# Kernel tuning notes

Measured on AMD Instinct MI355X. Metric: run time of the kernel, lower is better.

Reference implementation:

```python
import jax, jax.numpy as jnp
import numpy as np

NUM_ENT = 14541; NUM_REL = 237; NUM_EDGES = 544230
D = 200; B = 2048
IPERM = 1; IK_H = 20; IK_W = 10; NFILT = 96; KER = 9
FLAT = IK_H * 2 * IK_W * NFILT * IPERM
LEAKY = 0.2; EPS = 1e-5


def _chequer_perm(rng):
    # faithful reimplementation of RagatInteractE.get_chequer_perm
    ent_perm = np.stack([rng.permutation(D) for _ in range(IPERM)])
    rel_perm = np.stack([rng.permutation(D) for _ in range(IPERM)])
    comb = []
    for k in range(IPERM):
        temp = []; ei = 0; ri = 0
        for i in range(IK_H):
            for j in range(IK_W):
                ent_first = (k % 2 == 0) == (i % 2 == 0)
                if ent_first:
                    temp.append(ent_perm[k, ei]); ei += 1
                    temp.append(rel_perm[k, ri] + D); ri += 1
                else:
                    temp.append(rel_perm[k, ri] + D); ri += 1
                    temp.append(ent_perm[k, ei]); ei += 1
        comb.append(temp)
    return jnp.asarray(np.asarray(comb, dtype=np.int32))


def _bn1d(x, g, b):  # [N, C], training-mode batch stats (torch default)
    m = x.mean(0); v = x.var(0)
    return (x - m) / jnp.sqrt(v + EPS) * g + b


def _bn2d(x, g, b):  # [N, C, H, W]
    m = x.mean((0, 2, 3), keepdims=True); v = x.var((0, 2, 3), keepdims=True)
    return (x - m) / jnp.sqrt(v + EPS) * g[None, :, None, None] + b[None, :, None, None]


def _seg_softmax_agg(score, msg, seg, n):
    # segment softmax over edges grouped by destination node, then weighted scatter-add
    mx = jax.ops.segment_max(score, seg, num_segments=n)
    ex = jnp.exp(score - mx[seg])
    den = jax.ops.segment_sum(ex, seg, num_segments=n)
    alpha = ex / (den[seg] + 1e-16)
    return jax.ops.segment_sum(msg * alpha[:, None], seg, num_segments=n)


def setup_inputs() -> dict:
    key = jax.random.key(0)
    ks = jax.random.split(key, 20)
    f = lambda k, shp, s=0.1: jax.random.normal(k, shp, jnp.float32) * s
    rng = np.random.RandomState(0)
    return {
        'init_embed': f(ks[0], (NUM_ENT, D)),
        'init_rel': f(ks[1], (2 * NUM_REL, D)),
        'loop_rel': f(ks[2], (1, D)),
        'w_in': f(ks[3], (D, D)),
        'w_out': f(ks[4], (D, D)),
        'w_loop': f(ks[5], (D, D)),
        'w_rel': f(ks[6], (D, D)),
        'att_in': f(ks[7], (D,)),
        'att_out': f(ks[8], (D,)),
        'bn_conv_g': jnp.ones((D,), jnp.float32),
        'bn_conv_b': jnp.zeros((D,), jnp.float32),
        'conv_filt': f(ks[9], (NFILT, 1, KER, KER)),
        'bn0_g': jnp.ones((IPERM,), jnp.float32),
        'bn0_b': jnp.zeros((IPERM,), jnp.float32),
        'bn1_g': jnp.ones((NFILT * IPERM,), jnp.float32),
        'bn1_b': jnp.zeros((NFILT * IPERM,), jnp.float32),
        'fc_w': f(ks[10], (FLAT, D), 0.02),
        'fc_b': jnp.zeros((D,), jnp.float32),
        'bn2_g': jnp.ones((D,), jnp.float32),
        'bn2_b': jnp.zeros((D,), jnp.float32),
        'bias': jnp.zeros((NUM_ENT,), jnp.float32),
        'edge_index': jax.random.randint(ks[11], (2, NUM_EDGES), 0, NUM_ENT, jnp.int32),
        'edge_type': jnp.concatenate([
            jax.random.randint(ks[12], (NUM_EDGES // 2,), 0, NUM_REL, jnp.int32),
            jax.random.randint(ks[13], (NUM_EDGES // 2,), NUM_REL, 2 * NUM_REL, jnp.int32)]),
        'sub': jax.random.randint(ks[14], (B,), 0, NUM_ENT, jnp.int32),
        'rel': jax.random.randint(ks[15], (B,), 0, 2 * NUM_REL, jnp.int32),
        'chequer_perm': _chequer_perm(rng),
    }


def reference(init_embed, init_rel, loop_rel, w_in, w_out, w_loop, w_rel,
              att_in, att_out, bn_conv_g, bn_conv_b, conv_filt,
              bn0_g, bn0_b, bn1_g, bn1_b, fc_w, fc_b, bn2_g, bn2_b, bias,
              edge_index, edge_type, sub, rel, chequer_perm):
    # --- RagatConv (1 layer): relation-aware composition + edge attention + scatter-agg ---
    rel_full = jnp.concatenate([init_rel, loop_rel], 0)
    src, dst = edge_index[0], edge_index[1]
    comp = init_embed[dst] * rel_full[edge_type]          # [E, D] mult composition
    half = NUM_EDGES // 2
    msg_in = comp[:half] @ w_in                           # [E/2, D]
    msg_out = comp[half:] @ w_out
    s_in = jax.nn.leaky_relu((msg_in * att_in).sum(-1), LEAKY)
    s_out = jax.nn.leaky_relu((msg_out * att_out).sum(-1), LEAKY)
    agg_in = _seg_softmax_agg(s_in, msg_in, src[:half], NUM_ENT)
    agg_out = _seg_softmax_agg(s_out, msg_out, src[half:], NUM_ENT)
    loop_msg = (init_embed * loop_rel[0]) @ w_loop
    ent = (agg_in + agg_out + loop_msg) / 3.0
    ent = jnp.tanh(_bn1d(ent, bn_conv_g, bn_conv_b))      # [num_ent, D]
    rel_out = init_rel @ w_rel                            # [2*num_rel, D]

    # --- InteractE chequer-perm circular-conv scoring ---
    comb = jnp.concatenate([ent[sub], rel_out[rel]], 1)   # [B, 2D]
    cheq = comb[:, chequer_perm]                          # [B, IPERM, 2D]
    x = cheq.reshape(B, IPERM, 2 * IK_W, IK_H)
    x = _bn2d(x, bn0_g, bn0_b)
    p = KER // 2
    x = jnp.concatenate([x[..., -p:, :], x, x[..., :p, :]], axis=2)  # circular pad H
    x = jnp.concatenate([x[..., -p:], x, x[..., :p]], axis=3)        # circular pad W
    kern = jnp.tile(conv_filt, (IPERM, 1, 1, 1))          # [NFILT*IPERM, 1, K, K]
    x = jax.lax.conv_general_dilated(x, kern, (1, 1), 'VALID',
                                     dimension_numbers=('NCHW', 'OIHW', 'NCHW'),
                                     feature_group_count=IPERM)       # [B, 96, 20, 20]
    x = jax.nn.relu(_bn2d(x, bn1_g, bn1_b))
    x = x.reshape(B, FLAT)
    x = x @ fc_w + fc_b
    x = jax.nn.relu(_bn1d(x, bn2_g, bn2_b))               # [B, D]
    scores = x @ ent.T + bias                              # one_to_n scoring
    return jax.nn.sigmoid(scores)
```

## Files before the change

### kernel.cpp

```cpp
#include <hip/hip_runtime.h>
#include <hip/hip_bf16.h>

constexpr int DV     = 200;
constexpr int N_ENT  = 14541;
constexpr int N_EDGE = 544230;
constexpr int HALF_E = N_EDGE / 2;
constexpr int NSEG   = 2 * N_ENT;
constexpr int BB     = 2048;
constexpr int NF     = 96;
constexpr int FLATN  = 38400;
constexpr float LEAK = 0.2f;
constexpr float BEPS = 1e-5f;

typedef unsigned int u32;
typedef unsigned short u16;
typedef __attribute__((ext_vector_type(8))) short bf16x8;
typedef __attribute__((ext_vector_type(4))) float f32x4;
typedef __attribute__((ext_vector_type(4))) unsigned short u16x4;

constexpr size_t OFF_S    = 0;
constexpr size_t OFF_EID  = 544230;
constexpr size_t OFF_CNT  = 1088460;
constexpr size_t OFF_OFFS = 1117542;
constexpr size_t OFF_AGG  = 1146624;
constexpr size_t OFF_FC   = 6963218;
constexpr size_t ZERO_BEG = OFF_CNT;
constexpr size_t ZERO_END = OFF_FC + 409600;
constexpr size_t OFF_V    = 7372818;
constexpr size_t OFF_WTH  = 0;
constexpr size_t OFF_ENTH = 3840000;
constexpr size_t OFF_ENTL = 5352264;
constexpr size_t OFF_WTL  = 7373220;
constexpr size_t OFF_EMB  = 7373218;
constexpr size_t OFF_EPRE = 10281418;
constexpr size_t OFF_ENT  = 13189618;
constexpr size_t OFF_RELO = 16097818;
constexpr size_t OFF_CM   = 16192618;
constexpr size_t OFF_CV   = 16192818;
constexpr size_t OFF_CHEQ = 16193018;
constexpr size_t OFF_YH   = 16193020;
constexpr size_t OFF_YL   = 16406012;
constexpr size_t OFF_P0   = 17012218;
constexpr size_t OFF_ST0  = 17016314;
constexpr size_t OFF_CHP  = 17016316;
constexpr size_t OFF_B1SC = 17409532;
constexpr size_t OFF_B1BI = 17409628;
constexpr size_t OFF_XC   = 17819324;
constexpr size_t WS_WORDS = OFF_XC + 39321600;

__device__ inline float bf2f(u16 u) { return __uint_as_float(((u32)u) << 16); }
__device__ inline u16 f2bf(float f) {
    __hip_bfloat16 h = __float2bfloat16(f);
    return *reinterpret_cast<u16*>(&h);
}
__device__ inline void gl_lds16(const void* g, void* l) {
    __builtin_amdgcn_global_load_lds(
        (const __attribute__((address_space(1))) void*)g,
        (__attribute__((address_space(3))) void*)l, 16, 0, 0);
}

__global__ void k_vatt(const float* __restrict__ w_in, const float* __restrict__ w_out,
                       const float* __restrict__ att_in, const float* __restrict__ att_out,
                       float* __restrict__ v) {
    int t = blockIdx.x * 256 + threadIdx.x;
    if (t < DV) {
        float s = 0.f;
        for (int j = 0; j < DV; ++j) s += w_in[t * DV + j] * att_in[j];
        v[t] = s;
    } else if (t < 2 * DV) {
        int k = t - DV;
        float s = 0.f;
        for (int j = 0; j < DV; ++j) s += w_out[k * DV + j] * att_out[j];
        v[t] = s;
    }
}

__global__ void k_edge_score(const float* __restrict__ embed, const float* __restrict__ rel,
                             const int* __restrict__ eidx, const int* __restrict__ etype,
                             const float* __restrict__ v, float* __restrict__ s_all) {
    int gw = (blockIdx.x * 256 + threadIdx.x) >> 6;
    int lane = threadIdx.x & 63;
    if (gw >= N_EDGE) return;
    int e = gw;
    int dst = eidx[N_EDGE + e], et = etype[e];
    int dir = (e >= HALF_E);
    const float* vv = v + dir * DV;
    const float* er = embed + (size_t)dst * DV;
    const float* rr = rel + (size_t)et * DV;
    float acc = 0.f;
    for (int d = lane; d < DV; d += 64) acc += er[d] * rr[d] * vv[d];
    for (int off = 32; off > 0; off >>= 1) acc += __shfl_down(acc, off);
    if (lane == 0) {
        float s = acc > 0.f ? acc : LEAK * acc;
        s_all[e] = s;
    }
}

__global__ void k_hist(const int* __restrict__ eidx, u32* __restrict__ cnt) {
    int e = blockIdx.x * 256 + threadIdx.x;
    if (e >= N_EDGE) return;
    int seg = (e >= HALF_E ? N_ENT : 0) + eidx[e];
    atomicAdd(&cnt[seg], 1u);
}

__global__ void k_scan(u32* __restrict__ cnt, u32* __restrict__ offs) {
    __shared__ u32 s[256];
    __shared__ u32 base;
    if (threadIdx.x == 0) base = 0;
    __syncthreads();
    for (int c0 = 0; c0 < NSEG; c0 += 256) {
        int i = c0 + threadIdx.x;
        u32 vv = (i < NSEG) ? cnt[i] : 0;
        s[threadIdx.x] = vv;
        __syncthreads();
        for (int o = 1; o < 256; o <<= 1) {
            u32 t = (threadIdx.x >= (u32)o) ? s[threadIdx.x - o] : 0u;
            __syncthreads();
            s[threadIdx.x] += t;
            __syncthreads();
        }
        u32 exc = base + s[threadIdx.x] - vv;
        if (i < NSEG) { offs[i] = exc; cnt[i] = exc; }
        __syncthreads();
        if (threadIdx.x == 255) base += s[255];
        __syncthreads();
    }
}

__global__ void k_scatter(const int* __restrict__ eidx, u32* __restrict__ pos,
                          u32* __restrict__ eid) {
    int e = blockIdx.x * 256 + threadIdx.x;
    if (e >= N_EDGE) return;
    int seg = (e >= HALF_E ? N_ENT : 0) + eidx[e];
    u32 slot = atomicAdd(&pos[seg], 1u);
    eid[slot] = (u32)e;
}

__global__ void k_seg_agg(const float* __restrict__ embed, const float* __restrict__ rel,
                          const int* __restrict__ eidx, const int* __restrict__ etype,
                          const float* __restrict__ s_all, const u32* __restrict__ offs,
                          const u32* __restrict__ eid, float* __restrict__ aggC) {
    int gw = (blockIdx.x * 256 + threadIdx.x) >> 6;
    int lane = threadIdx.x & 63;
    if (gw >= NSEG) return;
    u32 beg = offs[gw];
    u32 end = (gw == NSEG - 1) ? (u32)N_EDGE : offs[gw + 1];
    int deg = (int)(end - beg);
    if (deg == 0) return;
    float m = -1e30f;
    for (int i = lane; i < deg; i += 64) m = fmaxf(m, s_all[eid[beg + i]]);
    for (int o = 32; o > 0; o >>= 1) m = fmaxf(m, __shfl_xor(m, o));
    float dsum = 0.f;
    for (int i = lane; i < deg; i += 64) dsum += expf(s_all[eid[beg + i]] - m);
    for (int o = 32; o > 0; o >>= 1) dsum += __shfl_xor(dsum, o);
    float inv = 1.f / (dsum + 1e-16f);
    float a0 = 0.f, a1 = 0.f, a2 = 0.f, a3 = 0.f;
    bool t3 = (lane < 8);
    for (int j = 0; j < deg; ++j) {
        int e = (int)eid[beg + j];
        float alpha = expf(s_all[e] - m) * inv;
        int dst = eidx[N_EDGE + e], et = etype[e];
        const float* er = embed + (size_t)dst * DV;
        const float* rr = rel + (size_t)et * DV;
        float p0 = er[lane] * rr[lane];
        float p1 = er[lane + 64] * rr[lane + 64];
        float p2 = er[lane + 128] * rr[lane + 128];
        float p3 = t3 ? er[lane + 192] * rr[lane + 192] : 0.f;
        a0 = fmaf(p0, alpha, a0);
        a1 = fmaf(p1, alpha, a1);
        a2 = fmaf(p2, alpha, a2);
        a3 = fmaf(p3, alpha, a3);
    }
    float* ag = aggC + (size_t)gw * DV;
    ag[lane] = a0;
    ag[lane + 64] = a1;
    ag[lane + 128] = a2;
    if (t3) ag[lane + 192] = a3;
}

__global__ void k_embloop(const float* __restrict__ embed, const float* __restrict__ lr,
                          float* __restrict__ outp) {
    size_t i = (size_t)blockIdx.x * 256 + threadIdx.x;
    if (i < (size_t)N_ENT * DV) outp[i] = embed[i] * lr[i % DV];
}

__global__ void gemm_nn(const float* __restrict__ A, const float* __restrict__ B,
                        float* __restrict__ C, int M, int N, int K, int beta) {
    __shared__ float As[16][65];
    __shared__ float Bs[16][64];
    int bm = blockIdx.x * 64, bn = blockIdx.y * 64;
    int tx = threadIdx.x & 15, ty = threadIdx.x >> 4;
    float acc[4][4] = {};
    for (int k0 = 0; k0 < K; k0 += 16) {
        for (int i = threadIdx.x; i < 1024; i += 256) {
            int m = i >> 4, k = i & 15;
            int gm = bm + m, gk = k0 + k;
            As[k][m] = (gm < M && gk < K) ? A[(size_t)gm * K + gk] : 0.f;
        }
        for (int i = threadIdx.x; i < 1024; i += 256) {
            int k = i >> 6, n = i & 63;
            int gk = k0 + k, gn = bn + n;
            Bs[k][n] = (gk < K && gn < N) ? B[(size_t)gk * N + gn] : 0.f;
        }
        __syncthreads();
#pragma unroll
        for (int k = 0; k < 16; ++k) {
            float a[4], bv[4];
#pragma unroll
            for (int i = 0; i < 4; i++) a[i] = As[k][ty * 4 + i];
#pragma unroll
            for (int j = 0; j < 4; j++) bv[j] = Bs[k][tx * 4 + j];
#pragma unroll
            for (int i = 0; i < 4; i++)
#pragma unroll
                for (int j = 0; j < 4; j++) acc[i][j] += a[i] * bv[j];
        }
        __syncthreads();
    }
#pragma unroll
    for (int i = 0; i < 4; i++) {
        int r = bm + ty * 4 + i;
        if (r >= M) continue;
#pragma unroll
        for (int j = 0; j < 4; j++) {
            int c = bn + tx * 4 + j;
            if (c >= N) continue;
            size_t idx = (size_t)r * N + c;
            C[idx] = beta ? C[idx] + acc[i][j] : acc[i][j];
        }
    }
}

__global__ void k_colstats(const float* __restrict__ X, int R,
                           float* __restrict__ cm, float* __restrict__ cv) {
    int col = blockIdx.x;
    __shared__ float rs[256], rss[256];
    float s = 0.f, ss = 0.f;
    for (int r = threadIdx.x; r < R; r += 256) {
        float x = X[(size_t)r * DV + col];
        s += x; ss += x * x;
    }
    rs[threadIdx.x] = s; rss[threadIdx.x] = ss;
    __syncthreads();
    for (int o = 128; o > 0; o >>= 1) {
        if (threadIdx.x < o) { rs[threadIdx.x] += rs[threadIdx.x + o]; rss[threadIdx.x] += rss[threadIdx.x + o]; }
        __syncthreads();
    }
    if (threadIdx.x == 0) {
        float m = rs[0] / R;
        cm[col] = m;
        cv[col] = rss[0] / R - m * m;
    }
}

__global__ void k_bn_ent(const float* __restrict__ epre, const float* __restrict__ cm,
                         const float* __restrict__ cv, const float* __restrict__ g,
                         const float* __restrict__ b, float* __restrict__ ent,
                         u16* __restrict__ eh, u16* __restrict__ el) {
    size_t i = (size_t)blockIdx.x * 256 + threadIdx.x;
    if (i >= (size_t)N_ENT * 208) return;
    int row = (int)(i / 208), col = (int)(i % 208);
    if (col < DV) {
        float val = (epre[(size_t)row * DV + col] - cm[col]) * rsqrtf(cv[col] + 9.f * BEPS) * g[col] + b[col];
        val = tanhf(val);
        ent[(size_t)row * DV + col] = val;
        u16 h = f2bf(val);
        eh[i] = h;
        el[i] = f2bf(val - bf2f(h));
    } else { eh[i] = 0; el[i] = 0; }
}

__global__ void k_bn2y(const float* __restrict__ fc, const float* __restrict__ cm,
                       const float* __restrict__ cv, const float* __restrict__ g,
                       const float* __restrict__ b, u16* __restrict__ yh,
                       u16* __restrict__ yl) {
    size_t i = (size_t)blockIdx.x * 256 + threadIdx.x;
    if (i >= (size_t)BB * 208) return;
    int row = (int)(i / 208), col = (int)(i % 208);
    if (col < DV) {
        float val = (fc[(size_t)row * DV + col] - cm[col]) * rsqrtf(cv[col] + BEPS) * g[col] + b[col];
        val = fmaxf(val, 0.f);
        u16 h = f2bf(val);
        yh[i] = h;
        yl[i] = f2bf(val - bf2f(h));
    } else { yh[i] = 0; yl[i] = 0; }
}

__global__ __launch_bounds__(256) void k_wt(const float* __restrict__ W,
                                            u16* __restrict__ Wth, u16* __restrict__ Wtl) {
    __shared__ float lds[64][65];
    int k0 = blockIdx.x * 64, n0 = blockIdx.y * 64;
    for (int idx = threadIdx.x; idx < 4096; idx += 256) {
        int kl = idx >> 6, nl = idx & 63;
        int gk = k0 + kl, gn = n0 + nl;
        lds[kl][nl] = (gn < DV) ? W[(size_t)gk * DV + gn] : 0.f;
    }
    __syncthreads();
    int nl = threadIdx.x >> 2, kq = threadIdx.x & 3;
    int gn = n0 + nl;
    if (gn >= DV) return;
    size_t base = (size_t)gn * FLATN + k0 + kq * 16;
    bf16x8 vh0, vh1, vl0, vl1;
#pragma unroll
    for (int j = 0; j < 8; ++j) {
        float w0 = lds[kq * 16 + j][nl];
        u16 h0 = f2bf(w0);
        vh0[j] = (short)h0; vl0[j] = (short)f2bf(w0 - bf2f(h0));
        float w1 = lds[kq * 16 + 8 + j][nl];
        u16 h1 = f2bf(w1);
        vh1[j] = (short)h1; vl1[j] = (short)f2bf(w1 - bf2f(h1));
    }
    *reinterpret_cast<bf16x8*>(Wth + base)     = vh0;
    *reinterpret_cast<bf16x8*>(Wth + base + 8) = vh1;
    *reinterpret_cast<bf16x8*>(Wtl + base)     = vl0;
    *reinterpret_cast<bf16x8*>(Wtl + base + 8) = vl1;
}

__global__ void k_cheq(const float* __restrict__ ent, const float* __restrict__ rel_out,
                       const int* __restrict__ sub, const int* __restrict__ rel,
                       const int* __restrict__ perm, float* __restrict__ cheq,
                       float* __restrict__ p0) {
    int b = blockIdx.x;
    int sb = sub[b], rb = rel[b];
    __shared__ float rs[256], rss[256];
    float s = 0.f, ss = 0.f;
    for (int i = threadIdx.x; i < 400; i += 256) {
        int p = perm[i];
        float v = (p < DV) ? ent[(size_t)sb * DV + p] : rel_out[(size_t)rb * DV + (p - DV)];
        cheq[(size_t)b * 400 + i] = v;
        s += v; ss += v * v;
    }
    rs[threadIdx.x] = s; rss[threadIdx.x] = ss;
    __syncthreads();
    for (int o = 128; o > 0; o >>= 1) {
        if (threadIdx.x < o) { rs[threadIdx.x] += rs[threadIdx.x + o]; rss[threadIdx.x] += rss[threadIdx.x + o]; }
        __syncthreads();
    }
    if (threadIdx.x == 0) { p0[b] = rs[0]; p0[BB + b] = rss[0]; }
}

__global__ void k_red_bn0(const float* __restrict__ p0, float* __restrict__ st) {
    __shared__ float rs[256], rss[256];
    float s = 0.f, ss = 0.f;
    for (int i = threadIdx.x; i < BB; i += 256) { s += p0[i]; ss += p0[BB + i]; }
    rs[threadIdx.x] = s; rss[threadIdx.x] = ss;
    __syncthreads();
    for (int o = 128; o > 0; o >>= 1) {
        if (threadIdx.x < o) { rs[threadIdx.x] += rs[threadIdx.x + o]; rss[threadIdx.x] += rss[threadIdx.x + o]; }
        __syncthreads();
    }
    if (threadIdx.x == 0) { st[0] = rs[0]; st[1] = rss[0]; }
}

__global__ __launch_bounds__(192, 3) void k_conv(const float* __restrict__ cheq,
                                              const float* __restrict__ st,
                                              const float* __restrict__ g0, const float* __restrict__ b0,
                                              const float* __restrict__ filt,
                                              __hip_bfloat16* __restrict__ xconv,
                                              float* __restrict__ chp) {
    int b = blockIdx.x, t = threadIdx.x;
    __shared__ float pad[784];
    __shared__ float flds[7968];
    __shared__ float red[192];
    for (int i = t; i < 7776; i += 192) {
        int f = i / 81, q = i - f * 81;
        flds[f * 83 + q] = filt[i];
    }
    const float N0 = (float)BB * 400.f;
    float m = st[0] / N0;
    float va = st[1] / N0 - m * m;
    float sg = rsqrtf(va + BEPS) * g0[0];
    float sb = b0[0] - m * sg;
    for (int i = t; i < 784; i += 192) {
        int h = i / 28, w = i % 28;
        int r = (h + 16) % 20, c = (w + 16) % 20;
        pad[i] = cheq[(size_t)b * 400 + r * 20 + c] * sg + sb;
    }
    __syncthreads();
    int f = t % 96, hp = t / 96;
    const float* fbase = flds + f * 83;
    float cs = 0.f, css = 0.f;
    u16* xo = (u16*)xconv + (size_t)b * FLATN + f * 400 + hp * 200;
    for (int rt = 0; rt < 10; ++rt) {
        int y = hp * 10 + rt;
        float acc[20];
#pragma unroll
        for (int x = 0; x < 20; ++x) acc[x] = 0.f;
        for (int dy = 0; dy < 9; ++dy) {
            float pr[28];
            const float4* prow = reinterpret_cast<const float4*>(&pad[(y + dy) * 28]);
#pragma unroll
            for (int qv = 0; qv < 7; ++qv) {
                float4 v4 = prow[qv];
                pr[qv * 4 + 0] = v4.x; pr[qv * 4 + 1] = v4.y;
                pr[qv * 4 + 2] = v4.z; pr[qv * 4 + 3] = v4.w;
            }
            float fw[9];
#pragma unroll
            for (int dx = 0; dx < 9; ++dx) fw[dx] = fbase[dy * 9 + dx];
#pragma unroll
            for (int dx = 0; dx < 9; ++dx)
#pragma unroll
                for (int x = 0; x < 20; ++x)
                    acc[x] = fmaf(pr[x + dx], fw[dx], acc[x]);
        }
#pragma unroll
        for (int x = 0; x < 20; ++x) { cs += acc[x]; css += acc[x] * acc[x]; }
#pragma unroll
        for (int jj = 0; jj < 5; ++jj) {
            u16x4 o;
#pragma unroll
            for (int q2 = 0; q2 < 4; ++q2) o[q2] = f2bf(acc[jj * 4 + q2]);
            *reinterpret_cast<u16x4*>(xo + rt * 20 + jj * 4) = o;
        }
    }
    red[t] = cs; __syncthreads();
    if (t < 96) chp[(size_t)b * 192 + t] = red[t] + red[t + 96];
    __syncthreads();
    red[t] = css; __syncthreads();
    if (t < 96) chp[(size_t)b * 192 + 96 + t] = red[t] + red[t + 96];
}

__global__ void k_bn1_final(const float* __restrict__ chp, const float* __restrict__ g1,
                            const float* __restrict__ b1, float* __restrict__ sc,
                            float* __restrict__ bi) {
    int c = blockIdx.x;
    __shared__ float rs[256], rss[256];
    float s = 0.f, ss = 0.f;
    for (int b = threadIdx.x; b < BB; b += 256) {
        s += chp[(size_t)b * 192 + c];
        ss += chp[(size_t)b * 192 + 96 + c];
    }
    rs[threadIdx.x] = s; rss[threadIdx.x] = ss;
    __syncthreads();
    for (int o = 128; o > 0; o >>= 1) {
        if (threadIdx.x < o) { rs[threadIdx.x] += rs[threadIdx.x + o]; rss[threadIdx.x] += rss[threadIdx.x + o]; }
        __syncthreads();
    }
    if (threadIdx.x == 0) {
        float N = (float)BB * 400.f;
        float m = rs[0] / N;
        float v = rss[0] / N - m * m;
        float s_ = rsqrtf(v + BEPS) * g1[c];
        sc[c] = s_;
        bi[c] = b1[c] - m * s_;
    }
}

__global__ __launch_bounds__(256) void k_fc_mfma(const u16* __restrict__ X,
        const u16* __restrict__ Wth, const u16* __restrict__ Wtl,
        const float* __restrict__ sc, const float* __restrict__ bi,
        float* __restrict__ outp) {
    __shared__ __align__(16) char blds[53248];
    int tid = threadIdx.x;
    int w = tid >> 6, lane = tid & 63;
    int lrow = lane & 15, lkg = lane >> 4;
    int mw = blockIdx.x * 128 + w * 32;
    int kbase = blockIdx.y * 1280;
    f32x4 acc[2][13] = {};
    for (int it = 0; it < 20; ++it) {
        int k0 = kbase + it * 64;
        __syncthreads();
        bf16x8 araw[2][2];
#pragma unroll
        for (int mf = 0; mf < 2; ++mf)
#pragma unroll
            for (int kt = 0; kt < 2; ++kt) {
                int r = mw + mf * 16 + lrow;
                int kk = k0 + kt * 32 + lkg * 8;
                araw[mf][kt] = *reinterpret_cast<const bf16x8*>(X + (size_t)r * FLATN + kk);
            }
#pragma unroll
        for (int q = 0; q < 7; ++q) {
            int bidx = q * 256 + w * 64;
            if (bidx < 1600) {
                int idx = bidx + lane;
                int n = idx >> 3;
                int slot = (idx & 7) ^ (n & 7);
                size_t gsrc = (size_t)n * FLATN + k0 + slot * 8;
                gl_lds16(Wth + gsrc, blds + bidx * 16);
                gl_lds16(Wtl + gsrc, blds + 26624 + bidx * 16);
            }
        }
        bf16x8 ah[2][2], al[2][2];
#pragma unroll
        for (int mf = 0; mf < 2; ++mf)
#pragma unroll
            for (int kt = 0; kt < 2; ++kt) {
                int kk = k0 + kt * 32 + lkg * 8;
                int c = kk / 400;
                float s_ = sc[c], b_ = bi[c];
                bf16x8 fh, fl;
#pragma unroll
                for (int j = 0; j < 8; ++j) {
                    float v = bf2f((u16)araw[mf][kt][j]);
                    v = fmaxf(fmaf(v, s_, b_), 0.f);
                    u16 h = f2bf(v);
                    fh[j] = (short)h;
                    fl[j] = (short)f2bf(v - bf2f(h));
                }
                ah[mf][kt] = fh;
                al[mf][kt] = fl;
            }
        __syncthreads();
#pragma unroll
        for (int nt = 0; nt < 13; ++nt) {
            int n = nt * 16 + lrow;
            int row = n * 128, nx = n & 7;
            int off0 = row + ((lkg ^ nx) << 4);
            int off1 = row + (((4 + lkg) ^ nx) << 4);
            bf16x8 bh0 = *reinterpret_cast<const bf16x8*>(blds + off0);
            bf16x8 bh1 = *reinterpret_cast<const bf16x8*>(blds + off1);
            bf16x8 bl0 = *reinterpret_cast<const bf16x8*>(blds + 26624 + off0);
            bf16x8 bl1 = *reinterpret_cast<const bf16x8*>(blds + 26624 + off1);
#pragma unroll
            for (int mf = 0; mf < 2; ++mf) {
                acc[mf][nt] = __builtin_amdgcn_mfma_f32_16x16x32_bf16(ah[mf][0], bh0, acc[mf][nt], 0, 0, 0);
                acc[mf][nt] = __builtin_amdgcn_mfma_f32_16x16x32_bf16(ah[mf][1], bh1, acc[mf][nt], 0, 0, 0);
                acc[mf][nt] = __builtin_amdgcn_mfma_f32_16x16x32_bf16(ah[mf][0], bl0, acc[mf][nt], 0, 0, 0);
                acc[mf][nt] = __builtin_amdgcn_mfma_f32_16x16x32_bf16(ah[mf][1], bl1, acc[mf][nt], 0, 0, 0);
                acc[mf][nt] = __builtin_amdgcn_mfma_f32_16x16x32_bf16(al[mf][0], bh0, acc[mf][nt], 0, 0, 0);
                acc[mf][nt] = __builtin_amdgcn_mfma_f32_16x16x32_bf16(al[mf][1], bh1, acc[mf][nt], 0, 0, 0);
            }
        }
    }
#pragma unroll
    for (int mf = 0; mf < 2; ++mf)
#pragma unroll
        for (int nt = 0; nt < 13; ++nt) {
            int col = nt * 16 + lrow;
            if (col < DV) {
#pragma unroll
                for (int i = 0; i < 4; ++i) {
                    int r = mw + mf * 16 + lkg * 4 + i;
                    unsafeAtomicAdd(&outp[(size_t)r * DV + col], acc[mf][nt][i]);
                }
            }
        }
}

__global__ __launch_bounds__(256) void k_sc_mfma(const u16* __restrict__ Yh, const u16* __restrict__ Yl,
        const u16* __restrict__ Eh, const u16* __restrict__ El,
        const float* __restrict__ bias, float* __restrict__ outp) {
    __shared__ __align__(16) char elds[32768];
    int tid = threadIdx.x;
    int w = tid >> 6, lane = tid & 63;
    int lrow = lane & 15, lkg = lane >> 4;
    int mw = blockIdx.x * 128 + w * 32;
    int bn = blockIdx.y * 256;
    f32x4 acc[2][16] = {};
    bf16x8 zv = {};
    for (int kt = 0; kt < 7; ++kt) {
        int kbase = kt * 32;
        __syncthreads();
        int kk = kbase + lkg * 8;
        bool kval = (kt < 6) || (lkg < 2);
        bf16x8 ah[2], al[2];
#pragma unroll
        for (int mf = 0; mf < 2; ++mf) {
            int r = mw + mf * 16 + lrow;
            size_t off = (size_t)r * 208 + kk;
            ah[mf] = kval ? *reinterpret_cast<const bf16x8*>(Yh + off) : zv;
            al[mf] = kval ? *reinterpret_cast<const bf16x8*>(Yl + off) : zv;
        }
#pragma unroll
        for (int q = 0; q < 4; ++q) {
            int bidx = q * 256 + w * 64;
            int idx = bidx + lane;
            int n = idx >> 2;
            int slot = (idx & 3) ^ (n & 3);
            int gn = bn + n; if (gn > N_ENT - 1) gn = N_ENT - 1;
            size_t gsrc = (size_t)gn * 208 + kbase + slot * 8;
            gl_lds16(Eh + gsrc, elds + bidx * 16);
            gl_lds16(El + gsrc, elds + 16384 + bidx * 16);
        }
        __syncthreads();
#pragma unroll
        for (int nt = 0; nt < 16; ++nt) {
            int n = nt * 16 + lrow;
            int off = n * 64 + ((lkg ^ (n & 3)) << 4);
            bf16x8 bh = *reinterpret_cast<const bf16x8*>(elds + off);
            bf16x8 bl = *reinterpret_cast<const bf16x8*>(elds + 16384 + off);
            acc[0][nt] = __builtin_amdgcn_mfma_f32_16x16x32_bf16(ah[0], bh, acc[0][nt], 0, 0, 0);
            acc[0][nt] = __builtin_amdgcn_mfma_f32_16x16x32_bf16(ah[0], bl, acc[0][nt], 0, 0, 0);
            acc[0][nt] = __builtin_amdgcn_mfma_f32_16x16x32_bf16(al[0], bh, acc[0][nt], 0, 0, 0);
            acc[1][nt] = __builtin_amdgcn_mfma_f32_16x16x32_bf16(ah[1], bh, acc[1][nt], 0, 0, 0);
            acc[1][nt] = __builtin_amdgcn_mfma_f32_16x16x32_bf16(ah[1], bl, acc[1][nt], 0, 0, 0);
            acc[1][nt] = __builtin_amdgcn_mfma_f32_16x16x32_bf16(al[1], bh, acc[1][nt], 0, 0, 0);
        }
    }
#pragma unroll
    for (int mf = 0; mf < 2; ++mf)
#pragma unroll
        for (int nt = 0; nt < 16; ++nt) {
            int col = bn + nt * 16 + lrow;
            if (col < N_ENT) {
                float bv = bias[col];
#pragma unroll
                for (int i = 0; i < 4; ++i) {
                    int r = mw + mf * 16 + lkg * 4 + i;
                    float s = acc[mf][nt][i] + bv;
                    outp[(size_t)r * N_ENT + col] = 1.f / (1.f + expf(-s));
                }
            }
        }
}

extern "C" void kernel_launch(void* const* d_in, const int* in_sizes, int n_in,
                              void* d_out, int out_size, void* d_ws, size_t ws_size,
                              hipStream_t stream) {
    const float* init_embed = (const float*)d_in[0];
    const float* init_rel   = (const float*)d_in[1];
    const float* loop_rel   = (const float*)d_in[2];
    const float* w_in   = (const float*)d_in[3];
    const float* w_out  = (const float*)d_in[4];
    const float* w_loop = (const float*)d_in[5];
    const float* w_rel  = (const float*)d_in[6];
    const float* att_in  = (const float*)d_in[7];
    const float* att_out = (const float*)d_in[8];
    const float* bnc_g = (const float*)d_in[9];
    const float* bnc_b = (const float*)d_in[10];
    const float* filt  = (const float*)d_in[11];
    const float* g0 = (const float*)d_in[12];
    const float* b0 = (const float*)d_in[13];
    const float* g1 = (const float*)d_in[14];
    const float* b1 = (const float*)d_in[15];
    const float* fc_w = (const float*)d_in[16];
    const float* g2 = (const float*)d_in[18];
    const float* b2 = (const float*)d_in[19];
    const float* bias = (const float*)d_in[20];
    const int* eidx  = (const int*)d_in[21];
    const int* etype = (const int*)d_in[22];
    const int* sub   = (const int*)d_in[23];
    const int* rel   = (const int*)d_in[24];
    const int* perm  = (const int*)d_in[25];

    float* ws = (float*)d_ws;
    float* outp = (float*)d_out;
    if (ws_size < WS_WORDS * sizeof(float)) return;

    float* s_all  = ws + OFF_S;
    u32*   eid    = (u32*)(ws + OFF_EID);
    u32*   cnt    = (u32*)(ws + OFF_CNT);
    u32*   offs   = (u32*)(ws + OFF_OFFS);
    float* aggC   = ws + OFF_AGG;
    float* fc_out = ws + OFF_FC;
    float* v      = ws + OFF_V;
    float* embl   = ws + OFF_EMB;
    float* epre   = ws + OFF_EPRE;
    float* ent    = ws + OFF_ENT;
    float* relo   = ws + OFF_RELO;
    float* cm     = ws + OFF_CM;
    float* cv     = ws + OFF_CV;
    float* cheq   = ws + OFF_CHEQ;
    float* p0     = ws + OFF_P0;
    float* st0    = ws + OFF_ST0;
    float* chp    = ws + OFF_CHP;
    float* b1sc   = ws + OFF_B1SC;
    float* b1bi   = ws + OFF_B1BI;
    u16*   Wth    = (u16*)(ws + OFF_WTH);
    u16*   Wtl    = (u16*)(ws + OFF_WTL);
    u16*   entH   = (u16*)(ws + OFF_ENTH);
    u16*   entL   = (u16*)(ws + OFF_ENTL);
    u16*   Yh     = (u16*)(ws + OFF_YH);
    u16*   Yl     = (u16*)(ws + OFF_YL);
    __hip_bfloat16* xconv = (__hip_bfloat16*)(ws + OFF_XC);

    hipMemsetAsync(ws + ZERO_BEG, 0, (ZERO_END - ZERO_BEG) * sizeof(float), stream);

    k_vatt<<<2, 256, 0, stream>>>(w_in, w_out, att_in, att_out, v);

    int edge_wave_blocks = (N_EDGE + 3) / 4;
    k_edge_score<<<edge_wave_blocks, 256, 0, stream>>>(init_embed, init_rel, eidx, etype, v, s_all);

    int eb = (N_EDGE + 255) / 256;
    k_hist<<<eb, 256, 0, stream>>>(eidx, cnt);
    k_scan<<<1, 256, 0, stream>>>(cnt, offs);
    k_scatter<<<eb, 256, 0, stream>>>(eidx, cnt, eid);
    k_seg_agg<<<(NSEG + 3) / 4, 256, 0, stream>>>(init_embed, init_rel, eidx, etype,
                                                  s_all, offs, eid, aggC);

    k_embloop<<<((size_t)N_ENT * DV + 255) / 256, 256, 0, stream>>>(init_embed, loop_rel, embl);

    dim3 gE((N_ENT + 63) / 64, (DV + 63) / 64);
    gemm_nn<<<gE, 256, 0, stream>>>(aggC,                       w_in,   epre, N_ENT, DV, DV, 0);
    gemm_nn<<<gE, 256, 0, stream>>>(aggC + (size_t)N_ENT * DV,  w_out,  epre, N_ENT, DV, DV, 1);
    gemm_nn<<<gE, 256, 0, stream>>>(embl,                       w_loop, epre, N_ENT, DV, DV, 1);
    dim3 gR((474 + 63) / 64, (DV + 63) / 64);
    gemm_nn<<<gR, 256, 0, stream>>>(init_rel, w_rel, relo, 474, DV, DV, 0);

    k_colstats<<<DV, 256, 0, stream>>>(epre, N_ENT, cm, cv);
    k_bn_ent<<<((size_t)N_ENT * 208 + 255) / 256, 256, 0, stream>>>(
        epre, cm, cv, bnc_g, bnc_b, ent, entH, entL);

    dim3 gW(FLATN / 64, 4);
    k_wt<<<gW, 256, 0, stream>>>(fc_w, Wth, Wtl);

    k_cheq<<<BB, 256, 0, stream>>>(ent, relo, sub, rel, perm, cheq, p0);
    k_red_bn0<<<1, 256, 0, stream>>>(p0, st0);
    k_conv<<<BB, 192, 0, stream>>>(cheq, st0, g0, b0, filt, xconv, chp);
    k_bn1_final<<<NF, 256, 0, stream>>>(chp, g1, b1, b1sc, b1bi);

    dim3 gFC(16, 30);
    k_fc_mfma<<<gFC, 256, 0, stream>>>((const u16*)xconv, Wth, Wtl, b1sc, b1bi, fc_out);

    k_colstats<<<DV, 256, 0, stream>>>(fc_out, BB, cm, cv);
    k_bn2y<<<((size_t)BB * 208 + 255) / 256, 256, 0, stream>>>(fc_out, cm, cv, g2, b2, Yh, Yl);

    dim3 gS(16, 57);
    k_sc_mfma<<<gS, 256, 0, stream>>>(Yh, Yl, entH, entL, bias, outp);
}
```

Measured before the change: 1.235 ms.

## Recast circular conv as im2col MFMA GEMM with split-bf16 precision

Replaces the scalar FP32 direct 9x9 convolution with an implicit-im2col GEMM on bf16 MFMA units. Each wave builds 16-pixel x 96-tap patches from the padded LDS tile, while the filters are stored in LDS as hi/lo bf16 pairs padded to 96 taps. Three MFMAs per product (hi*hi, lo*hi, hi*lo) keep accuracy close to fp32. The block grows to 256 threads, and channel statistics are reduced with shuffles plus an LDS sum. The cost is extra bf16 splitting work, padding-waste MFMAs, and uneven work across waves (7 vs 6 m-tiles).

```diff
diff --git a/kernel.cpp b/kernel.cpp
--- a/kernel.cpp
+++ b/kernel.cpp
@@ -352,73 +352,130 @@
     if (threadIdx.x == 0) { st[0] = rs[0]; st[1] = rss[0]; }
 }
 
-__global__ __launch_bounds__(192, 3) void k_conv(const float* __restrict__ cheq,
+__global__ __launch_bounds__(256) void k_conv(const float* __restrict__ cheq,
                                               const float* __restrict__ st,
                                               const float* __restrict__ g0, const float* __restrict__ b0,
                                               const float* __restrict__ filt,
                                               __hip_bfloat16* __restrict__ xconv,
                                               float* __restrict__ chp) {
-    int b = blockIdx.x, t = threadIdx.x;
+    int t = threadIdx.x, b = blockIdx.x;
     __shared__ float pad[784];
-    __shared__ float flds[7968];
-    __shared__ float red[192];
-    for (int i = t; i < 7776; i += 192) {
+    __shared__ u16 fh[96 * 104];
+    __shared__ u16 fl[96 * 104];
+    __shared__ float sred[4][192];
+    const float N0 = (float)BB * 400.f;
+    float m0 = st[0] / N0;
+    float va = st[1] / N0 - m0 * m0;
+    float sg = rsqrtf(va + BEPS) * g0[0];
+    float sb = b0[0] - m0 * sg;
+    for (int i = t; i < 7776; i += 256) {
         int f = i / 81, q = i - f * 81;
-        flds[f * 83 + q] = filt[i];
-    }
-    const float N0 = (float)BB * 400.f;
-    float m = st[0] / N0;
-    float va = st[1] / N0 - m * m;
-    float sg = rsqrtf(va + BEPS) * g0[0];
-    float sb = b0[0] - m * sg;
-    for (int i = t; i < 784; i += 192) {
-        int h = i / 28, w = i % 28;
-        int r = (h + 16) % 20, c = (w + 16) % 20;
+        float wv = filt[i];
+        u16 h = f2bf(wv);
+        fh[f * 104 + q] = h;
+        fl[f * 104 + q] = f2bf(wv - bf2f(h));
+    }
+    for (int i = t; i < 96 * 15; i += 256) {
+        int f = i / 15, q = 81 + i % 15;
+        fh[f * 104 + q] = 0; fl[f * 104 + q] = 0;
+    }
+    for (int i = t; i < 784; i += 256) {
+        int h = i / 28, w2 = i % 28;
+        int r = (h + 16) % 20, c = (w2 + 16) % 20;
         pad[i] = cheq[(size_t)b * 400 + r * 20 + c] * sg + sb;
     }
     __syncthreads();
-    int f = t % 96, hp = t / 96;
-    const float* fbase = flds + f * 83;
-    float cs = 0.f, css = 0.f;
-    u16* xo = (u16*)xconv + (size_t)b * FLATN + f * 400 + hp * 200;
-    for (int rt = 0; rt < 10; ++rt) {
-        int y = hp * 10 + rt;
-        float acc[20];
-#pragma unroll
-        for (int x = 0; x < 20; ++x) acc[x] = 0.f;
-        for (int dy = 0; dy < 9; ++dy) {
-            float pr[28];
-            const float4* prow = reinterpret_cast<const float4*>(&pad[(y + dy) * 28]);
-#pragma unroll
-            for (int qv = 0; qv < 7; ++qv) {
-                float4 v4 = prow[qv];
-                pr[qv * 4 + 0] = v4.x; pr[qv * 4 + 1] = v4.y;
-                pr[qv * 4 + 2] = v4.z; pr[qv * 4 + 3] = v4.w;
-            }
-            float fw[9];
-#pragma unroll
-            for (int dx = 0; dx < 9; ++dx) fw[dx] = fbase[dy * 9 + dx];
-#pragma unroll
-            for (int dx = 0; dx < 9; ++dx)
-#pragma unroll
-                for (int x = 0; x < 20; ++x)
-                    acc[x] = fmaf(pr[x + dx], fw[dx], acc[x]);
-        }
-#pragma unroll
-        for (int x = 0; x < 20; ++x) { cs += acc[x]; css += acc[x] * acc[x]; }
-#pragma unroll
-        for (int jj = 0; jj < 5; ++jj) {
+    int w = t >> 6, lane = t & 63;
+    int lrow = lane & 15, lkg = lane >> 4;
+    int mfBeg = (w == 0) ? 0 : (1 + 6 * w);
+    int mfEnd = mfBeg + ((w == 0) ? 7 : 6);
+    float cs[6] = {}, css[6] = {};
+    u16* xb = (u16*)xconv + (size_t)b * FLATN;
+    for (int mf = mfBeg; mf < mfEnd; mf += 2) {
+        bool two = (mf + 1 < mfEnd);
+        bf16x8 ah[2][3], al[2][3];
+#pragma unroll
+        for (int im = 0; im < 2; ++im) {
+            int mfi = (im && !two) ? mf : (mf + im);
+            int p = mfi * 16 + lrow;
+            int y = p / 20, x = p - (p / 20) * 20;
+            int pb = y * 28 + x;
+#pragma unroll
+            for (int ks = 0; ks < 3; ++ks) {
+                bf16x8 vh, vl;
+#pragma unroll
+                for (int j = 0; j < 8; ++j) {
+                    int k = ks * 32 + lkg * 8 + j;
+                    int dy = (k * 57) >> 9;
+                    int dx = k - 9 * dy;
+                    float v = (ks < 2 || k < 81) ? pad[pb + dy * 28 + dx] : 0.f;
+                    u16 h = f2bf(v);
+                    vh[j] = (short)h;
+                    vl[j] = (short)f2bf(v - bf2f(h));
+                }
+                ah[im][ks] = vh; al[im][ks] = vl;
+            }
+        }
+        f32x4 acc0[6] = {}, acc1[6] = {};
+#pragma unroll
+        for (int nt = 0; nt < 6; ++nt) {
+            int fb = (nt * 16 + lrow) * 104;
+#pragma unroll
+            for (int ks = 0; ks < 3; ++ks) {
+                bf16x8 bh = *reinterpret_cast<const bf16x8*>(fh + fb + ks * 32 + lkg * 8);
+                bf16x8 bl = *reinterpret_cast<const bf16x8*>(fl + fb + ks * 32 + lkg * 8);
+                acc0[nt] = __builtin_amdgcn_mfma_f32_16x16x32_bf16(ah[0][ks], bh, acc0[nt], 0, 0, 0);
+                acc0[nt] = __builtin_amdgcn_mfma_f32_16x16x32_bf16(al[0][ks], bh, acc0[nt], 0, 0, 0);
+                acc0[nt] = __builtin_amdgcn_mfma_f32_16x16x32_bf16(ah[0][ks], bl, acc0[nt], 0, 0, 0);
+                if (two) {
+                    acc1[nt] = __builtin_amdgcn_mfma_f32_16x16x32_bf16(ah[1][ks], bh, acc1[nt], 0, 0, 0);
+                    acc1[nt] = __builtin_amdgcn_mfma_f32_16x16x32_bf16(al[1][ks], bh, acc1[nt], 0, 0, 0);
+                    acc1[nt] = __builtin_amdgcn_mfma_f32_16x16x32_bf16(ah[1][ks], bl, acc1[nt], 0, 0, 0);
+                }
+            }
+        }
+#pragma unroll
+        for (int nt = 0; nt < 6; ++nt) {
+            int f = nt * 16 + lrow;
+            int p0 = mf * 16 + lkg * 4;
             u16x4 o;
 #pragma unroll
-            for (int q2 = 0; q2 < 4; ++q2) o[q2] = f2bf(acc[jj * 4 + q2]);
-            *reinterpret_cast<u16x4*>(xo + rt * 20 + jj * 4) = o;
-        }
-    }
-    red[t] = cs; __syncthreads();
-    if (t < 96) chp[(size_t)b * 192 + t] = red[t] + red[t + 96];
+            for (int i = 0; i < 4; ++i) {
+                float v = acc0[nt][i];
+                cs[nt] += v; css[nt] += v * v;
+                o[i] = f2bf(v);
+            }
+            *reinterpret_cast<u16x4*>(xb + f * 400 + p0) = o;
+            if (two) {
+                int p1 = (mf + 1) * 16 + lkg * 4;
+                u16x4 o1;
+#pragma unroll
+                for (int i = 0; i < 4; ++i) {
+                    float v = acc1[nt][i];
+                    cs[nt] += v; css[nt] += v * v;
+                    o1[i] = f2bf(v);
+                }
+                *reinterpret_cast<u16x4*>(xb + f * 400 + p1) = o1;
+            }
+        }
+    }
+#pragma unroll
+    for (int nt = 0; nt < 6; ++nt) {
+        cs[nt] += __shfl_xor(cs[nt], 16);  cs[nt] += __shfl_xor(cs[nt], 32);
+        css[nt] += __shfl_xor(css[nt], 16); css[nt] += __shfl_xor(css[nt], 32);
+    }
+    if (lane < 16) {
+#pragma unroll
+        for (int nt = 0; nt < 6; ++nt) {
+            sred[w][nt * 16 + lane] = cs[nt];
+            sred[w][96 + nt * 16 + lane] = css[nt];
+        }
+    }
     __syncthreads();
-    red[t] = css; __syncthreads();
-    if (t < 96) chp[(size_t)b * 192 + 96 + t] = red[t] + red[t + 96];
+    if (t < 192) {
+        float sum = sred[0][t] + sred[1][t] + sred[2][t] + sred[3][t];
+        chp[(size_t)b * 192 + t] = sum;
+    }
 }
 
 __global__ void k_bn1_final(const float* __restrict__ chp, const float* __restrict__ g1,
@@ -490,17 +547,17 @@
                 int kk = k0 + kt * 32 + lkg * 8;
                 int c = kk / 400;
                 float s_ = sc[c], b_ = bi[c];
-                bf16x8 fh, fl;
+                bf16x8 fh2, fl2;
 #pragma unroll
                 for (int j = 0; j < 8; ++j) {
                     float v = bf2f((u16)araw[mf][kt][j]);
                     v = fmaxf(fmaf(v, s_, b_), 0.f);
                     u16 h = f2bf(v);
-                    fh[j] = (short)h;
-                    fl[j] = (short)f2bf(v - bf2f(h));
+                    fh2[j] = (short)h;
+                    fl2[j] = (short)f2bf(v - bf2f(h));
                 }
-                ah[mf][kt] = fh;
-                al[mf][kt] = fl;
+                ah[mf][kt] = fh2;
+                al[mf][kt] = fl2;
             }
         __syncthreads();
 #pragma unroll
@@ -698,7 +755,7 @@
 
     k_cheq<<<BB, 256, 0, stream>>>(ent, relo, sub, rel, perm, cheq, p0);
     k_red_bn0<<<1, 256, 0, stream>>>(p0, st0);
-    k_conv<<<BB, 192, 0, stream>>>(cheq, st0, g0, b0, filt, xconv, chp);
+    k_conv<<<BB, 256, 0, stream>>>(cheq, st0, g0, b0, filt, xconv, chp);
     k_bn1_final<<<NF, 256, 0, stream>>>(chp, g1, b1, b1sc, b1bi);
 
     dim3 gFC(16, 30);
```

After: 1.249 ms. No clear change (+1.1%).
